# Performance work log

Measured on AMD Instinct MI355X. Metric: run time of the kernel, lower is better.

## Reference

```python
import jax, jax.numpy as jnp
import numpy as np

N, E = 50000, 800000
DIN, DH, DOUT, L = 128, 256, 64, 4


def setup_inputs() -> dict:
    key = jax.random.key(0)
    ks = jax.random.split(key, 8)
    x = jax.random.normal(ks[0], (N, DIN), dtype=jnp.float32)
    edge_index = jax.random.randint(ks[1], (2, E), 0, N, dtype=jnp.int64 if jax.config.jax_enable_x64 else jnp.int32)
    W_emb = jax.random.normal(ks[2], (DIN, DH), dtype=jnp.float32) / np.float32(np.sqrt(DIN))
    b_emb = jnp.zeros((DH,), jnp.float32)
    W_conv = jax.random.normal(ks[3], (L, DH, DH), dtype=jnp.float32) / np.float32(np.sqrt(DH))
    b_conv = jnp.zeros((L, DH), jnp.float32)
    W_out = jax.random.normal(ks[4], (DH, DOUT), dtype=jnp.float32) / np.float32(np.sqrt(DH))
    b_out = jnp.zeros((DOUT,), jnp.float32)
    return {"x": x, "edge_index": edge_index, "W_emb": W_emb, "b_emb": b_emb,
            "W_conv": W_conv, "b_conv": b_conv, "W_out": W_out, "b_out": b_out}


def _gcn_layer(h, src, dst, norm, W, b, n):
    # GCNConv: transform, then sym-normalized neighbor aggregation, then bias
    h = h @ W                                  # [N, DH]
    msg = h[src] * norm[:, None]               # [E+N, DH] gather + scale
    return jax.ops.segment_sum(msg, dst, num_segments=n) + b


def reference(x, edge_index, W_emb, b_emb, W_conv, b_conv, W_out, b_out):
    n = x.shape[0]
    loop = jnp.arange(n, dtype=edge_index.dtype)
    src = jnp.concatenate([edge_index[0], loop])   # add self-loops (PyG default)
    dst = jnp.concatenate([edge_index[1], loop])
    deg = jax.ops.segment_sum(jnp.ones_like(src, dtype=x.dtype), dst, num_segments=n)
    dinv = jnp.where(deg > 0, jax.lax.rsqrt(deg), jnp.zeros_like(deg))
    norm = dinv[src] * dinv[dst]                   # per-edge D^-1/2 A D^-1/2 weight
    h = x @ W_emb + b_emb                          # embedding (no activation)
    for i in range(L):                             # small fixed layer count
        h = jnp.tanh(_gcn_layer(h, src, dst, norm, W_conv[i], b_conv[i], n))
    return h @ W_out + b_out
```

## Files before the change

### kernel.cpp

```cpp
#include <hip/hip_runtime.h>
#include <math.h>

#define N_NODES 50000
#define N_EDGES 800000
#define DIN 128
#define DH 256
#define DOUT 64
#define NLAYERS 4

typedef unsigned short u16;
typedef __attribute__((ext_vector_type(8))) _Float16 half8;
typedef __attribute__((ext_vector_type(4))) float f32x4;

__device__ inline u16 f2h(float f) {
  _Float16 h = (_Float16)f;
  return *(u16*)&h;
}
__device__ inline float h2f(u16 u) {
  _Float16 h = *(_Float16*)&u;
  return (float)h;
}
__device__ inline int invp(int j) {
  int s = j >> 6, t = j & 63;
  return s * 64 + (t & 3) * 16 + (t >> 2);
}

#define GLD16(gp, lp)                                                        \
  __builtin_amdgcn_global_load_lds(                                          \
      (const __attribute__((address_space(1))) void*)(const void*)(gp),      \
      (__attribute__((address_space(3))) void*)(void*)(lp), 16, 0, 0)


__global__ void k_scan1(const int* __restrict__ cnt, int* __restrict__ rowptr,
                        int* __restrict__ bsum, float* __restrict__ dinv, int n) {
  __shared__ int sm[256];
  int i = blockIdx.x * 256 + threadIdx.x;
  int v = (i < n) ? cnt[i] : 0;
  if (i < n) dinv[i] = rsqrtf((float)v + 1.0f);
  sm[threadIdx.x] = v;
  __syncthreads();
  for (int off = 1; off < 256; off <<= 1) {
    int t = (threadIdx.x >= off) ? sm[threadIdx.x - off] : 0;
    __syncthreads();
    sm[threadIdx.x] += t;
    __syncthreads();
  }
  if (i < n) rowptr[i + 1] = sm[threadIdx.x];
  if (threadIdx.x == 255) bsum[blockIdx.x] = sm[255];
}

__global__ void k_scan2(int* bsum, int nb) {
  __shared__ int sm[256];
  int v = (threadIdx.x < nb) ? bsum[threadIdx.x] : 0;
  sm[threadIdx.x] = v;
  __syncthreads();
  for (int off = 1; off < 256; off <<= 1) {
    int t = (threadIdx.x >= off) ? sm[threadIdx.x - off] : 0;
    __syncthreads();
    sm[threadIdx.x] += t;
    __syncthreads();
  }
  if (threadIdx.x < nb) bsum[threadIdx.x] = sm[threadIdx.x] - v;
}

__global__ void k_scan3(int* __restrict__ rowptr, const int* __restrict__ bsum,
                        int* __restrict__ cursor, int n) {
  int i = blockIdx.x * 256 + threadIdx.x;
  if (i < n) {
    int v = rowptr[i + 1] + bsum[blockIdx.x];
    rowptr[i + 1] = v;
    if (i + 1 < n) cursor[i + 1] = v;
  }
  if (blockIdx.x == 0 && threadIdx.x == 0) {
    rowptr[0] = 0;
    cursor[0] = 0;
  }
}

__global__ void k_fill(const int* __restrict__ src, const int* __restrict__ dst,
                       const float* __restrict__ dinv,
                       int* __restrict__ cursor, int2* __restrict__ csr, int e) {
  int i = blockIdx.x * blockDim.x + threadIdx.x;
  if (i < e) {
    int d = dst[i], s = src[i];
    int pos = atomicAdd(&cursor[d], 1);
    csr[pos] = make_int2(s, __float_as_int(dinv[s] * dinv[d]));
  }
}

#define X_Q (N_NODES * DIN / 4)
#define W_EMB_SZ (DIN * DH)
#define W_CONV_SZ (DH * DH)
#define W_OUT_SZ (3 * DH * DOUT)
#define W_TOT (W_EMB_SZ + 4 * W_CONV_SZ + W_OUT_SZ)
#define B_TOT (DH + 4 * DH)

__global__ void k_convert(const float* __restrict__ x, u16* __restrict__ x_f16,
                          const float* __restrict__ W_emb, const float* __restrict__ W_conv,
                          const float* __restrict__ W_out,
                          const float* __restrict__ b_emb, const float* __restrict__ b_conv,
                          u16* __restrict__ Bt_emb, u16* __restrict__ Bt_conv,
                          u16* __restrict__ Bt_out,
                          float* __restrict__ bEmbP, float* __restrict__ bConvP,
                          const int* __restrict__ edst, int* __restrict__ cnt) {
  int i = blockIdx.x * 256 + threadIdx.x;
  if (i < X_Q) {
    float4 v = ((const float4*)x)[i];
    ushort4 o;
    o.x = f2h(v.x); o.y = f2h(v.y); o.z = f2h(v.z); o.w = f2h(v.w);
    ((ushort4*)x_f16)[i] = o;
    return;
  }
  int t = i - X_Q;
  if (t < W_EMB_SZ) {
    int n = t >> 7, k = t & (DIN - 1);
    Bt_emb[t] = f2h(W_emb[k * DH + n]);
  } else if (t < W_EMB_SZ + 4 * W_CONV_SZ) {
    int j = t - W_EMB_SZ;
    int l = j >> 16, jj = j & (W_CONV_SZ - 1);
    int n = jj >> 8, k2 = jj & (DH - 1);
    Bt_conv[j] = f2h(W_conv[l * W_CONV_SZ + invp(k2) * DH + n]);
  } else if (t < W_TOT) {
    int j = t - W_EMB_SZ - 4 * W_CONV_SZ;
    int n = j / (3 * DH), kp = j % (3 * DH);
    int s0 = kp >> 8, k2 = kp & (DH - 1);
    float wv = W_out[invp(k2) * DOUT + n];
    u16 hiv = f2h(wv);
    u16 v = hiv;
    if (s0 == 1) v = f2h(wv - h2f(hiv));
    Bt_out[j] = v;
  } else {
    int t2 = t - W_TOT;
    if (t2 < B_TOT) {
      if (t2 < DH) bEmbP[t2] = b_emb[invp(t2)];
      else {
        int j = t2 - DH, l = j >> 8, jj = j & (DH - 1);
        bConvP[j] = b_conv[l * DH + invp(jj)];
      }
    } else {
      int t3 = t2 - B_TOT;
      if (t3 < N_EDGES) atomicAdd(&cnt[edst[t3]], 1);
    }
  }
}

template <int BN, int NSPLIT, int EPI>
__global__ __launch_bounds__(256) void k_gemm_mfma(
    const u16* __restrict__ Ahi, const u16* __restrict__ Alo,
    const u16* __restrict__ Bt, const float* __restrict__ bias,
    float* __restrict__ Cf, u16* __restrict__ Cb, int M, int K, int N) {
  constexpr int BM = 128, BK = 64;
  constexpr int WN = BN / 2;
  constexpr int NT = WN / 16;
  __shared__ u16 As[2 * 8 * 512];
  const int tid = threadIdx.x;
  const int w = tid >> 6, lane = tid & 63;
  const int q = lane >> 4, r = lane & 15;
  const int wmg = (w >> 1) * 4;
  const int wn = (w & 1) * WN;
  const int m0 = blockIdx.x * BM, n0 = blockIdx.y * BN;
  const int Kp = NSPLIT * K;
  const int srow = lane & 15;
  const int sk = (lane >> 4) * 8;

  f32x4 acc[4][NT];
#pragma unroll
  for (int t = 0; t < 4; t++)
#pragma unroll
    for (int u = 0; u < NT; u++) acc[t][u] = (f32x4){0.f, 0.f, 0.f, 0.f};

  for (int k0 = 0; k0 < Kp; k0 += BK) {
    const u16* Aptr;
    int ka;
    if (NSPLIT == 1) {
      Aptr = Ahi; ka = k0;
    } else {
      Aptr = (k0 < 2 * K) ? Ahi : Alo;
      ka = (k0 < K) ? k0 : ((k0 < 2 * K) ? (k0 - K) : (k0 - 2 * K));
    }
#pragma unroll
    for (int ii = 0; ii < 4; ii++) {
      int g = w * 2 + (ii & 1), kb = ii >> 1;
      int grow = m0 + g * 16 + srow;
      if (grow > M - 1) grow = M - 1;
      const u16* gp = Aptr + (size_t)grow * K + ka + kb * 32 + sk;
      GLD16(gp, &As[(kb * 8 + g) * 512] + (size_t)lane * 8);
    }
    __syncthreads();
#pragma unroll
    for (int kb = 0; kb < 2; kb++) {
      half8 af[4], bfr[NT];
#pragma unroll
      for (int u = 0; u < NT; u++)
        bfr[u] = *(const half8*)(Bt + (size_t)(n0 + wn + u * 16 + r) * Kp +
                                 k0 + kb * 32 + q * 8);
#pragma unroll
      for (int t = 0; t < 4; t++)
        af[t] = *(const half8*)&As[((kb * 8 + wmg + t) * 64 + lane) * 8];
#pragma unroll
      for (int t = 0; t < 4; t++)
#pragma unroll
        for (int u = 0; u < NT; u++)
          acc[t][u] = __builtin_amdgcn_mfma_f32_16x16x32_f16(af[t], bfr[u], acc[t][u], 0, 0, 0);
    }
    __syncthreads();
  }

  if (EPI == 1) {
    int cb = n0 + wn;
    float4 bp = bias ? *(const float4*)(bias + cb + r * 4)
                     : make_float4(0.f, 0.f, 0.f, 0.f);
#pragma unroll
    for (int t = 0; t < 4; t++) {
#pragma unroll
      for (int rg = 0; rg < 4; rg++) {
        int row = m0 + (w >> 1) * 64 + t * 16 + q * 4 + rg;
        if (row < M) {
          ushort4 o;
          o.x = f2h(acc[t][0][rg] + bp.x);
          o.y = f2h(acc[t][1][rg] + bp.y);
          o.z = f2h(acc[t][2][rg] + bp.z);
          o.w = f2h(acc[t][3][rg] + bp.w);
          *(ushort4*)(Cb + (size_t)row * N + cb + r * 4) = o;
        }
      }
    }
  } else {
    float bv[NT];
#pragma unroll
    for (int u = 0; u < NT; u++) bv[u] = bias ? bias[n0 + wn + u * 16 + r] : 0.f;
#pragma unroll
    for (int t = 0; t < 4; t++) {
#pragma unroll
      for (int rg = 0; rg < 4; rg++) {
        int row = m0 + (w >> 1) * 64 + t * 16 + q * 4 + rg;
        if (row < M) {
#pragma unroll
          for (int u = 0; u < NT; u++) {
            int col = n0 + wn + u * 16 + r;
            Cf[(size_t)row * N + col] = acc[t][u][rg] + bv[u];
          }
        }
      }
    }
  }
}

__global__ void k_aggregate(const u16* __restrict__ tmph,
                            const int* __restrict__ rowptr, const int2* __restrict__ csr,
                            const float* __restrict__ dinv, const float* __restrict__ bias,
                            u16* __restrict__ hi, u16* __restrict__ lo, int n) {
  int i = (int)((blockIdx.x * (size_t)blockDim.x + threadIdx.x) >> 6);
  int lane = threadIdx.x & 63;
  if (i >= n) return;
  float w0 = dinv[i];
  w0 *= w0;
  const ushort4* T = (const ushort4*)tmph;
  float4 bv = ((const float4*)bias)[lane];
  ushort4 t0 = T[(size_t)i * 64 + lane];
  float ax = bv.x + w0 * h2f(t0.x);
  float ay = bv.y + w0 * h2f(t0.y);
  float az = bv.z + w0 * h2f(t0.z);
  float aw = bv.w + w0 * h2f(t0.w);
  int s = rowptr[i], e = rowptr[i + 1];
  int j = s;
  for (; j + 8 <= e; j += 8) {
    int2 c[8];
    ushort4 v[8];
#pragma unroll
    for (int u = 0; u < 8; u++) c[u] = csr[j + u];
#pragma unroll
    for (int u = 0; u < 8; u++) v[u] = T[(size_t)c[u].x * 64 + lane];
#pragma unroll
    for (int u = 0; u < 8; u++) {
      float f = __int_as_float(c[u].y);
      ax += f * h2f(v[u].x);
      ay += f * h2f(v[u].y);
      az += f * h2f(v[u].z);
      aw += f * h2f(v[u].w);
    }
  }
  for (; j + 4 <= e; j += 4) {
    int2 c[4];
    ushort4 v[4];
#pragma unroll
    for (int u = 0; u < 4; u++) c[u] = csr[j + u];
#pragma unroll
    for (int u = 0; u < 4; u++) v[u] = T[(size_t)c[u].x * 64 + lane];
#pragma unroll
    for (int u = 0; u < 4; u++) {
      float f = __int_as_float(c[u].y);
      ax += f * h2f(v[u].x);
      ay += f * h2f(v[u].y);
      az += f * h2f(v[u].z);
      aw += f * h2f(v[u].w);
    }
  }
  for (; j < e; j++) {
    int2 c = csr[j];
    ushort4 v = T[(size_t)c.x * 64 + lane];
    float f = __int_as_float(c.y);
    ax += f * h2f(v.x);
    ay += f * h2f(v.y);
    az += f * h2f(v.z);
    aw += f * h2f(v.w);
  }
  float ox = tanhf(ax), oy = tanhf(ay), oz = tanhf(az), ow = tanhf(aw);
  size_t base = (size_t)i * DH + lane * 4;
  ushort4 hv;
  hv.x = f2h(ox); hv.y = f2h(oy); hv.z = f2h(oz); hv.w = f2h(ow);
  *(ushort4*)(hi + base) = hv;
  if (lo) {
    ushort4 lv;
    lv.x = f2h(ox - h2f(hv.x));
    lv.y = f2h(oy - h2f(hv.y));
    lv.z = f2h(oz - h2f(hv.z));
    lv.w = f2h(ow - h2f(hv.w));
    *(ushort4*)(lo + base) = lv;
  }
}


extern "C" void kernel_launch(void* const* d_in, const int* in_sizes, int n_in,
                              void* d_out, int out_size, void* d_ws, size_t ws_size,
                              hipStream_t stream) {
  const float* x = (const float*)d_in[0];
  const int* eidx = (const int*)d_in[1];
  const int* esrc = eidx;
  const int* edst = eidx + N_EDGES;
  const float* W_emb = (const float*)d_in[2];
  const float* b_emb = (const float*)d_in[3];
  const float* W_conv = (const float*)d_in[4];
  const float* b_conv = (const float*)d_in[5];
  const float* W_out = (const float*)d_in[6];
  const float* b_out = (const float*)d_in[7];
  float* out = (float*)d_out;

  char* ws = (char*)d_ws;
  size_t off = 0;
  auto alloc = [&](size_t bytes) -> void* {
    void* p = ws + off;
    off += (bytes + 255) & ~(size_t)255;
    return p;
  };
  u16* tmph = (u16*)alloc((size_t)N_NODES * DH * 2);
  u16* h_hi = (u16*)alloc((size_t)N_NODES * DH * 2);
  u16* h_lo = (u16*)alloc((size_t)N_NODES * DH * 2);
  u16* x_f16 = h_lo;
  float* dinv = (float*)alloc((size_t)N_NODES * 4);
  int* cnt = (int*)alloc((size_t)N_NODES * 4);
  int* rowptr = (int*)alloc((size_t)(N_NODES + 1) * 4);
  int* cursor = (int*)alloc((size_t)N_NODES * 4);
  int* bsum = (int*)alloc((size_t)((N_NODES + 255) / 256) * 4);
  int2* csr = (int2*)alloc((size_t)N_EDGES * 8);
  u16* Bt_emb = (u16*)alloc((size_t)W_EMB_SZ * 2);
  u16* Bt_conv = (u16*)alloc((size_t)4 * W_CONV_SZ * 2);
  u16* Bt_out = (u16*)alloc((size_t)W_OUT_SZ * 2);
  float* bEmbP = (float*)alloc((size_t)DH * 4);
  float* bConvP = (float*)alloc((size_t)4 * DH * 4);

  int nb = (N_NODES + 255) / 256;
  int eb = (N_EDGES + 255) / 256;

  hipMemsetAsync(cnt, 0, (size_t)N_NODES * 4, stream);
  {
    int tot = X_Q + W_TOT + B_TOT + N_EDGES;
    k_convert<<<(tot + 255) / 256, 256, 0, stream>>>(x, x_f16, W_emb, W_conv, W_out,
                                                     b_emb, b_conv, Bt_emb, Bt_conv,
                                                     Bt_out, bEmbP, bConvP, edst, cnt);
  }
  k_scan1<<<nb, 256, 0, stream>>>(cnt, rowptr, bsum, dinv, N_NODES);
  k_scan2<<<1, 256, 0, stream>>>(bsum, nb);
  k_scan3<<<nb, 256, 0, stream>>>(rowptr, bsum, cursor, N_NODES);
  k_fill<<<eb, 256, 0, stream>>>(esrc, edst, dinv, cursor, csr, N_EDGES);

  int mblocks = (N_NODES + 127) / 128;
  int aggblocks = (N_NODES * 64 + 255) / 256;

  {
    dim3 g(mblocks, DH / 128);
    k_gemm_mfma<128, 1, 1><<<g, 256, 0, stream>>>(x_f16, nullptr, Bt_emb, bEmbP,
                                                  nullptr, h_hi, N_NODES, DIN, DH);
  }
  for (int l = 0; l < NLAYERS; l++) {
    dim3 g(mblocks, DH / 128);
    k_gemm_mfma<128, 1, 1><<<g, 256, 0, stream>>>(h_hi, nullptr,
                                                  Bt_conv + (size_t)l * W_CONV_SZ, nullptr,
                                                  nullptr, tmph, N_NODES, DH, DH);
    k_aggregate<<<aggblocks, 256, 0, stream>>>(tmph, rowptr, csr, dinv,
                                               bConvP + (size_t)l * DH,
                                               h_hi, (l == 3) ? h_lo : nullptr, N_NODES);
  }
  {
    dim3 g(mblocks, 1);
    k_gemm_mfma<64, 3, 0><<<g, 256, 0, stream>>>(h_hi, h_lo, Bt_out, b_out,
                                                 out, nullptr, N_NODES, DH, DOUT);
  }
}
```

Measured before the change: 563.0 us.

## Split aggregation across feature slices with 8 lanes per node and nontemporal CSR access

Each node's 256-wide feature row is now split into 8 column slices handled by separate blocks. Each slice is covered by 8 lanes, so a wave processes 8 nodes instead of one. The intent is to shrink the per-block gather working set so the tmph table stays in cache, and to raise memory-level parallelism across nodes. CSR entries are read, and outputs written, with nontemporal hints to avoid polluting cache. The trade-off is that CSR indices are re-read 8 times (once per slice), each gather becomes only 64 bytes per node per wave, and the unroll drops from 8 to 4.

```diff
diff --git a/kernel.cpp b/kernel.cpp
--- a/kernel.cpp
+++ b/kernel.cpp
@@ -9,6 +9,7 @@
 #define NLAYERS 4
 
 typedef unsigned short u16;
+typedef unsigned long long u64;
 typedef __attribute__((ext_vector_type(8))) _Float16 half8;
 typedef __attribute__((ext_vector_type(4))) float f32x4;
 
@@ -250,73 +251,61 @@
                             const int* __restrict__ rowptr, const int2* __restrict__ csr,
                             const float* __restrict__ dinv, const float* __restrict__ bias,
                             u16* __restrict__ hi, u16* __restrict__ lo, int n) {
-  int i = (int)((blockIdx.x * (size_t)blockDim.x + threadIdx.x) >> 6);
-  int lane = threadIdx.x & 63;
+  int slice = blockIdx.x & 7;
+  int grp = blockIdx.x >> 3;
+  int slot = threadIdx.x >> 3;
+  int fl = threadIdx.x & 7;
+  int i = grp * 32 + slot;
   if (i >= n) return;
+  int co = slice * 8 + fl;
+  const ushort4* T = (const ushort4*)tmph;
   float w0 = dinv[i];
   w0 *= w0;
-  const ushort4* T = (const ushort4*)tmph;
-  float4 bv = ((const float4*)bias)[lane];
-  ushort4 t0 = T[(size_t)i * 64 + lane];
+  float4 bv = ((const float4*)bias)[co];
+  ushort4 t0 = T[(size_t)i * 64 + co];
   float ax = bv.x + w0 * h2f(t0.x);
   float ay = bv.y + w0 * h2f(t0.y);
   float az = bv.z + w0 * h2f(t0.z);
   float aw = bv.w + w0 * h2f(t0.w);
   int s = rowptr[i], e = rowptr[i + 1];
+  const u64* C = (const u64*)csr;
   int j = s;
-  for (; j + 8 <= e; j += 8) {
-    int2 c[8];
-    ushort4 v[8];
-#pragma unroll
-    for (int u = 0; u < 8; u++) c[u] = csr[j + u];
-#pragma unroll
-    for (int u = 0; u < 8; u++) v[u] = T[(size_t)c[u].x * 64 + lane];
-#pragma unroll
-    for (int u = 0; u < 8; u++) {
-      float f = __int_as_float(c[u].y);
-      ax += f * h2f(v[u].x);
-      ay += f * h2f(v[u].y);
-      az += f * h2f(v[u].z);
-      aw += f * h2f(v[u].w);
-    }
-  }
   for (; j + 4 <= e; j += 4) {
-    int2 c[4];
-    ushort4 v[4];
-#pragma unroll
-    for (int u = 0; u < 4; u++) c[u] = csr[j + u];
-#pragma unroll
-    for (int u = 0; u < 4; u++) v[u] = T[(size_t)c[u].x * 64 + lane];
-#pragma unroll
-    for (int u = 0; u < 4; u++) {
-      float f = __int_as_float(c[u].y);
-      ax += f * h2f(v[u].x);
-      ay += f * h2f(v[u].y);
-      az += f * h2f(v[u].z);
-      aw += f * h2f(v[u].w);
-    }
+    u64 c0 = __builtin_nontemporal_load(C + j);
+    u64 c1 = __builtin_nontemporal_load(C + j + 1);
+    u64 c2 = __builtin_nontemporal_load(C + j + 2);
+    u64 c3 = __builtin_nontemporal_load(C + j + 3);
+    ushort4 v0 = T[(size_t)(unsigned)(c0 & 0xffffffffu) * 64 + co];
+    ushort4 v1 = T[(size_t)(unsigned)(c1 & 0xffffffffu) * 64 + co];
+    ushort4 v2 = T[(size_t)(unsigned)(c2 & 0xffffffffu) * 64 + co];
+    ushort4 v3 = T[(size_t)(unsigned)(c3 & 0xffffffffu) * 64 + co];
+    float f0 = __uint_as_float((unsigned)(c0 >> 32));
+    float f1 = __uint_as_float((unsigned)(c1 >> 32));
+    float f2 = __uint_as_float((unsigned)(c2 >> 32));
+    float f3 = __uint_as_float((unsigned)(c3 >> 32));
+    ax += f0 * h2f(v0.x); ay += f0 * h2f(v0.y); az += f0 * h2f(v0.z); aw += f0 * h2f(v0.w);
+    ax += f1 * h2f(v1.x); ay += f1 * h2f(v1.y); az += f1 * h2f(v1.z); aw += f1 * h2f(v1.w);
+    ax += f2 * h2f(v2.x); ay += f2 * h2f(v2.y); az += f2 * h2f(v2.z); aw += f2 * h2f(v2.w);
+    ax += f3 * h2f(v3.x); ay += f3 * h2f(v3.y); az += f3 * h2f(v3.z); aw += f3 * h2f(v3.w);
   }
   for (; j < e; j++) {
-    int2 c = csr[j];
-    ushort4 v = T[(size_t)c.x * 64 + lane];
-    float f = __int_as_float(c.y);
-    ax += f * h2f(v.x);
-    ay += f * h2f(v.y);
-    az += f * h2f(v.z);
-    aw += f * h2f(v.w);
+    u64 c = __builtin_nontemporal_load(C + j);
+    ushort4 v = T[(size_t)(unsigned)(c & 0xffffffffu) * 64 + co];
+    float f = __uint_as_float((unsigned)(c >> 32));
+    ax += f * h2f(v.x); ay += f * h2f(v.y); az += f * h2f(v.z); aw += f * h2f(v.w);
   }
   float ox = tanhf(ax), oy = tanhf(ay), oz = tanhf(az), ow = tanhf(aw);
-  size_t base = (size_t)i * DH + lane * 4;
+  size_t base = (size_t)i * DH + (size_t)co * 4;
   ushort4 hv;
   hv.x = f2h(ox); hv.y = f2h(oy); hv.z = f2h(oz); hv.w = f2h(ow);
-  *(ushort4*)(hi + base) = hv;
+  __builtin_nontemporal_store(*(u64*)&hv, (u64*)(hi + base));
   if (lo) {
     ushort4 lv;
     lv.x = f2h(ox - h2f(hv.x));
     lv.y = f2h(oy - h2f(hv.y));
     lv.z = f2h(oz - h2f(hv.z));
     lv.w = f2h(ow - h2f(hv.w));
-    *(ushort4*)(lo + base) = lv;
+    __builtin_nontemporal_store(*(u64*)&lv, (u64*)(lo + base));
   }
 }
 
@@ -375,7 +364,7 @@
   k_fill<<<eb, 256, 0, stream>>>(esrc, edst, dinv, cursor, csr, N_EDGES);
 
   int mblocks = (N_NODES + 127) / 128;
-  int aggblocks = (N_NODES * 64 + 255) / 256;
+  int aggblocks = ((N_NODES + 31) / 32) * 8;
 
   {
     dim3 g(mblocks, DH / 128);
```

Result: slower. 858.9 us (+52.6%).
